# Kernel optimization log

Measured on AMD Instinct MI355X. Metric: run time of the kernel, lower is better.

Reference implementation:

```python
import jax, jax.numpy as jnp
import numpy as np


def setup_inputs() -> dict:
    key = jax.random.key(0)
    ks = jax.random.split(key, 8)
    B, T, V, D, H, C = 1024, 80, 50000, 300, 300, 3
    sent = jax.random.randint(ks[0], (B, T), 0, V, dtype=jnp.int32)
    lens = jax.random.randint(ks[1], (B,), 1, T + 1, dtype=jnp.int32)
    emb = jax.random.normal(ks[2], (V, D), dtype=jnp.float32) * 0.1
    Wx = jax.random.normal(ks[3], (D, 4 * H), dtype=jnp.float32) * 0.05
    Wh = jax.random.normal(ks[4], (H, 4 * H), dtype=jnp.float32) * 0.05
    b = jnp.zeros((4 * H,), dtype=jnp.float32)
    Wout = jax.random.normal(ks[5], (H, C), dtype=jnp.float32) * 0.05
    bout = jnp.zeros((C,), dtype=jnp.float32)
    return {"sent": sent, "lens": lens, "emb": emb, "Wx": Wx, "Wh": Wh,
            "b": b, "Wout": Wout, "bout": bout}


def _lstm_masked(x, mask, Wx, Wh, b, H):
    # x: [B, T, D], mask: [B, T] float. Scan over time keeping h,c in carry.
    B = x.shape[0]
    h0 = jnp.zeros((B, H), dtype=x.dtype)
    c0 = jnp.zeros((B, H), dtype=x.dtype)

    def step(carry, inp):
        h, c = carry
        xt, mt = inp                      # xt: [B, D], mt: [B]
        gates = xt @ Wx + h @ Wh + b      # [B, 4H]
        i, f, g, o = jnp.split(gates, 4, axis=-1)
        i, f, o = jax.nn.sigmoid(i), jax.nn.sigmoid(f), jax.nn.sigmoid(o)
        g = jnp.tanh(g)
        c_new = f * c + i * g
        h_new = o * jnp.tanh(c_new)
        m = mt[:, None]
        h = m * h_new + (1.0 - m) * h     # mask-based state blending
        c = m * c_new + (1.0 - m) * c
        return (h, c), None

    xs = (jnp.swapaxes(x, 0, 1), jnp.swapaxes(mask, 0, 1))  # time-major
    (h, c), _ = jax.lax.scan(step, (h0, c0), xs)
    return h


def reference(sent, lens, emb, Wx, Wh, b, Wout, bout):
    T = sent.shape[1]
    H = Wh.shape[0]
    x = emb[sent]                                         # [B, T, D]
    mask = (jnp.arange(T)[None, :] < lens[:, None]).astype(x.dtype)  # [B, T]
    h = _lstm_masked(x, mask, Wx, Wh, b, H)
    logit = h @ Wout + bout                               # [B, C]
    return logit
```

## Files before the change

### kernel.cpp

```cpp
#include <hip/hip_runtime.h>
#include <hip/hip_fp16.h>


typedef float    f32x4 __attribute__((ext_vector_type(4)));
typedef _Float16 f16;
typedef _Float16 f16x8 __attribute__((ext_vector_type(8)));
typedef unsigned long long u64;
typedef unsigned int       u32;

#define NB    1024
#define TT    80
#define NV    50000
#define ND    300
#define KP    320
#define NKT   10
#define SL    75
#define SLP   80
#define NTPG  5
#define NTIL  20
#define TPB   256
#define GRID  256

#define OFF_EMB   0
#define OFF_WHP   32000000
#define OFF_WXP   32819200
#define OFF_HBUF  33638400
#define HBUF_SZ   (NB * KP)
#define OFF_HF32  34949120
#define OFF_FLAGS 36177920
#define WS_NEED   36182016

__global__ __launch_bounds__(256) void absa_prep_emb(
    const float* __restrict__ emb, f16* __restrict__ embb) {
  int i = blockIdx.x * 256 + threadIdx.x;
  if (i >= NV * KP / 8) return;
  int flat = i * 8;
  int row  = flat / KP;
  int k    = flat - row * KP;
  f16x8 o;
  if (k + 7 < ND) {
    float4 a = *reinterpret_cast<const float4*>(emb + row * ND + k);
    float4 b = *reinterpret_cast<const float4*>(emb + row * ND + k + 4);
    o[0] = (f16)a.x; o[1] = (f16)a.y; o[2] = (f16)a.z; o[3] = (f16)a.w;
    o[4] = (f16)b.x; o[5] = (f16)b.y; o[6] = (f16)b.z; o[7] = (f16)b.w;
  } else {
#pragma unroll
    for (int e = 0; e < 8; ++e) {
      int kk = k + e;
      float v = (kk < ND) ? emb[row * ND + kk] : (kk == ND ? 1.0f : 0.0f);
      o[e] = (f16)v;
    }
  }
  *reinterpret_cast<f16x8*>(embb + flat) = o;
}

__global__ __launch_bounds__(256) void absa_prep_pack(
    const float* __restrict__ W, const float* __restrict__ bias,
    f16* __restrict__ out, int mode) {
  int idx = blockIdx.x * 256 + threadIdx.x;
  if (idx >= 4 * NTIL * NKT * 512) return;
  int e    = idx & 7;
  int lane = (idx >> 3) & 63;
  int fid  = idx >> 9;
  int kt   = fid % NKT;
  int rem  = fid / NKT;
  int nt   = rem % NTIL;
  int n    = rem / NTIL;
  int gi   = nt / NTPG, ti = nt - gi * NTPG;
  int k    = kt * 32 + (lane >> 4) * 8 + e;
  int cc   = ti * 16 + (lane & 15);
  float v = 0.f;
  if (cc < SL) {
    int col = gi * 300 + n * SL + cc;
    if (mode == 0) {
      if (k < ND)       v = W[k * 1200 + col];
      else if (k == ND) v = bias[col];
    } else {
      int kl = k % SLP, n2 = k / SLP;
      if (kl < SL)      v = W[(n2 * SL + kl) * 1200 + col];
    }
  }
  out[idx] = (f16)v;
}

__device__ __forceinline__ float sigf(float x) {
  return __builtin_amdgcn_rcpf(1.f + __builtin_amdgcn_exp2f(-1.44269504f * x));
}
__device__ __forceinline__ float tanhf_(float x) {
  float xx = fminf(15.f, fmaxf(-15.f, x));
  return 1.f - 2.f * __builtin_amdgcn_rcpf(1.f + __builtin_amdgcn_exp2f(2.88539008f * xx));
}

__global__ __launch_bounds__(TPB, 1) void absa_lstm(
    const int* __restrict__ sent, const int* __restrict__ lens,
    const f16* __restrict__ embb,
    const f16* __restrict__ whp, const f16* __restrict__ wxp,
    f16* __restrict__ hbuf, float* __restrict__ hf32,
    int* __restrict__ flags) {
  const int bid = blockIdx.x;
  const int s   = bid & 7;
  const int q   = bid >> 3;
  const int n   = q & 3;
  const int g   = s * 8 + (q >> 2);

  const int tid = threadIdx.x;
  const int w   = tid >> 6;
  const int l   = tid & 63;
  const int l15 = l & 15, lk = l >> 4;
  const int grow0 = g * 16;

  __shared__ float gates[4 * 80 * 20];
  __shared__ float c_lds[80 * 20];
  __shared__ float hf_lds[80 * 20];
  __shared__ int   sent_lds[16 * TT];
  __shared__ int   len_lds[16];

  for (int i = tid; i < 16 * TT; i += TPB) sent_lds[i] = sent[g * (16 * TT) + i];
  if (tid < 16) len_lds[tid] = lens[grow0 + tid];
  for (int i = tid; i < 80 * 20; i += TPB) { c_lds[i] = 0.f; hf_lds[i] = 0.f; }
  __syncthreads();

  int maxlen = 0;
#pragma unroll
  for (int r = 0; r < 16; ++r) maxlen = max(maxlen, len_lds[r]);

  f16x8 wh[NTPG][NKT], wx[NTPG][NKT];
#pragma unroll
  for (int j = 0; j < NTPG; ++j) {
#pragma unroll
    for (int kt = 0; kt < NKT; ++kt) {
      int off = ((n * NTIL + (w * NTPG + j)) * NKT + kt) * 512 + l * 8;
      wh[j][kt] = *reinterpret_cast<const f16x8*>(whp + off);
      wx[j][kt] = *reinterpret_cast<const f16x8*>(wxp + off);
    }
  }

  int gaddr[NTPG];
#pragma unroll
  for (int j = 0; j < NTPG; ++j)
    gaddr[j] = ((w * 80) + j * 16 + l15) * 20 + lk * 4;

  int* const flagp = flags + g * 16;

  for (int t = 0; t < TT; ++t) {
    if (t >= maxlen) break;

    f32x4 acc[NTPG];
#pragma unroll
    for (int j = 0; j < NTPG; ++j) acc[j] = (f32x4){0.f, 0.f, 0.f, 0.f};
    {
      f16x8 xa[NKT];
      const int srow = sent_lds[l15 * TT + t];
#pragma unroll
      for (int kt = 0; kt < NKT; ++kt)
        xa[kt] = *reinterpret_cast<const f16x8*>(embb + srow * KP + kt * 32 + lk * 8);
#pragma unroll
      for (int j = 0; j < NTPG; ++j)
#pragma unroll
        for (int kt = 0; kt < NKT; ++kt)
          acc[j] = __builtin_amdgcn_mfma_f32_16x16x32_f16(xa[kt], wx[j][kt], acc[j], 0, 0, 0);
    }

    if (t > 0) {
      {
        const int target = 4 * t;
        int spins = 0;
        while (__hip_atomic_load(flagp, __ATOMIC_RELAXED, __HIP_MEMORY_SCOPE_AGENT) < target
               && ++spins < (1 << 22))
          __builtin_amdgcn_s_sleep(1);
      }
      const f16* hp = hbuf + ((t - 1) & 1) * HBUF_SZ + (grow0 + l15) * KP;
      f16x8 ha[NKT];
#pragma unroll
      for (int kt = 0; kt < NKT; ++kt) {
        union { u64 qd[2]; f16x8 v; } u;
        const u64* p = reinterpret_cast<const u64*>(hp + kt * 32 + lk * 8);
        u.qd[0] = __hip_atomic_load(p,     __ATOMIC_RELAXED, __HIP_MEMORY_SCOPE_AGENT);
        u.qd[1] = __hip_atomic_load(p + 1, __ATOMIC_RELAXED, __HIP_MEMORY_SCOPE_AGENT);
        ha[kt] = u.v;
      }
#pragma unroll
      for (int j = 0; j < NTPG; ++j)
#pragma unroll
        for (int kt = 0; kt < NKT; ++kt)
          acc[j] = __builtin_amdgcn_mfma_f32_16x16x32_f16(ha[kt], wh[j][kt], acc[j], 0, 0, 0);
    }

#pragma unroll
    for (int j = 0; j < NTPG; ++j)
      *reinterpret_cast<f32x4*>(&gates[gaddr[j]]) = acc[j];
    __syncthreads();

    f16* hc = hbuf + (t & 1) * HBUF_SZ;
    for (int i = tid; i < 16 * 38; i += TPB) {
      int row = i & 15;
      int cc0 = (i >> 4) * 2;
      float hv[2];
#pragma unroll
      for (int e = 0; e < 2; ++e) {
        int cc = cc0 + e;
        float h = 0.f;
        if (cc < SL) {
          int base = cc * 20 + row;
          if (t < len_lds[row]) {
            float vi = gates[(0 * 80 + cc) * 20 + row];
            float vf = gates[(1 * 80 + cc) * 20 + row];
            float vg = gates[(2 * 80 + cc) * 20 + row];
            float vo = gates[(3 * 80 + cc) * 20 + row];
            float iv = sigf(vi), fv = sigf(vf), ov = sigf(vo);
            float gv = tanhf_(vg);
            float cn = fv * c_lds[base] + iv * gv;
            h = ov * tanhf_(cn);
            c_lds[base] = cn;
            hf_lds[base] = h;
          } else {
            h = hf_lds[base];
          }
        }
        hv[e] = h;
      }
      union { f16 h2[2]; u32 uu; } pu;
      pu.h2[0] = (f16)hv[0]; pu.h2[1] = (f16)hv[1];
      u32* dst = reinterpret_cast<u32*>(hc + (grow0 + row) * KP + n * SLP + cc0);
      __hip_atomic_store(dst, pu.uu, __ATOMIC_RELAXED, __HIP_MEMORY_SCOPE_AGENT);
    }
    __syncthreads();
    if (tid == 0)
      __hip_atomic_fetch_add(flagp, 1, __ATOMIC_RELAXED, __HIP_MEMORY_SCOPE_AGENT);
  }

  for (int i = tid; i < 16 * SL; i += TPB) {
    int row = i & 15, cc = i >> 4;
    hf32[(grow0 + row) * ND + n * SL + cc] = hf_lds[cc * 20 + row];
  }
}

__global__ __launch_bounds__(256) void absa_logits(
    const float* __restrict__ hf32, const float* __restrict__ Wout,
    const float* __restrict__ bout, float* __restrict__ out) {
  int row = blockIdx.x * 256 + threadIdx.x;
  if (row >= NB) return;
  float s0 = bout[0], s1 = bout[1], s2 = bout[2];
  for (int k = 0; k < ND; ++k) {
    float h = hf32[row * ND + k];
    s0 += h * Wout[k * 3 + 0];
    s1 += h * Wout[k * 3 + 1];
    s2 += h * Wout[k * 3 + 2];
  }
  out[row * 3 + 0] = s0;
  out[row * 3 + 1] = s1;
  out[row * 3 + 2] = s2;
}

extern "C" void kernel_launch(void* const* d_in, const int* in_sizes, int n_in,
                              void* d_out, int out_size, void* d_ws, size_t ws_size,
                              hipStream_t stream) {
  const int*   sent = (const int*)d_in[0];
  const int*   lens = (const int*)d_in[1];
  const float* emb  = (const float*)d_in[2];
  const float* Wx   = (const float*)d_in[3];
  const float* Wh   = (const float*)d_in[4];
  const float* bv   = (const float*)d_in[5];
  const float* Wout = (const float*)d_in[6];
  const float* bout = (const float*)d_in[7];
  float* out = (float*)d_out;

  char* wsb = (char*)d_ws;
  f16*   embb  = (f16*)(wsb + OFF_EMB);
  f16*   whp   = (f16*)(wsb + OFF_WHP);
  f16*   wxp   = (f16*)(wsb + OFF_WXP);
  f16*   hbuf  = (f16*)(wsb + OFF_HBUF);
  float* hf32  = (float*)(wsb + OFF_HF32);
  int*   flags = (int*)(wsb + OFF_FLAGS);

  (void)hipMemsetAsync(hbuf, 0, 2 * HBUF_SZ * 2, stream);
  (void)hipMemsetAsync(flags, 0, 64 * 64, stream);

  absa_prep_emb <<<(NV * KP / 8 + 255) / 256, 256, 0, stream>>>(emb, embb);
  absa_prep_pack<<<4 * NTIL * NKT * 512 / 256, 256, 0, stream>>>(Wh, bv, whp, 1);
  absa_prep_pack<<<4 * NTIL * NKT * 512 / 256, 256, 0, stream>>>(Wx, bv, wxp, 0);
  absa_lstm     <<<GRID, TPB, 0, stream>>>(sent, lens, embb, whp, wxp, hbuf, hf32, flags);
  absa_logits   <<<NB / 256, 256, 0, stream>>>(hf32, Wout, bout, out);
}
```

Before: 655.9 us.

## Replace flag counter sync with tagged h-buffer slabs and prefetch next x-projection

Removes the per-group atomic flag counter and instead embeds a step tag in the low mantissa bit of each f16 h value. Consumers spin directly on the data they need across 8 rotating buffer slabs, and gates are double-buffered in LDS so the second barrier per step can be dropped. The input projection for step t+1 is computed after h is published, taking it off the critical path, and Wx is now streamed from memory each step instead of held in registers. The two weight-pack launches are merged, and the logits kernel becomes a wave-per-row reduction. The tag bits slightly perturb h precision, and rereading Wx adds memory traffic.

```diff
diff --git a/kernel.cpp b/kernel.cpp
--- a/kernel.cpp
+++ b/kernel.cpp
@@ -20,15 +20,17 @@
 #define NTIL  20
 #define TPB   256
 #define GRID  256
+#define NSLAB 8
+
+#define TAGMASK 0x0001000100010001ULL
 
 #define OFF_EMB   0
 #define OFF_WHP   32000000
 #define OFF_WXP   32819200
 #define OFF_HBUF  33638400
 #define HBUF_SZ   (NB * KP)
-#define OFF_HF32  34949120
-#define OFF_FLAGS 36177920
-#define WS_NEED   36182016
+#define OFF_HF32  38881280
+#define WS_NEED   40110080
 
 __global__ __launch_bounds__(256) void absa_prep_emb(
     const float* __restrict__ emb, f16* __restrict__ embb) {
@@ -54,11 +56,15 @@
   *reinterpret_cast<f16x8*>(embb + flat) = o;
 }
 
-__global__ __launch_bounds__(256) void absa_prep_pack(
-    const float* __restrict__ W, const float* __restrict__ bias,
-    f16* __restrict__ out, int mode) {
-  int idx = blockIdx.x * 256 + threadIdx.x;
-  if (idx >= 4 * NTIL * NKT * 512) return;
+__global__ __launch_bounds__(256) void absa_prep_pack2(
+    const float* __restrict__ Wx, const float* __restrict__ Wh,
+    const float* __restrict__ bias,
+    f16* __restrict__ wxp, f16* __restrict__ whp) {
+  const int half = 4 * NTIL * NKT * 512;
+  int idx0 = blockIdx.x * 256 + threadIdx.x;
+  if (idx0 >= 2 * half) return;
+  int mode = idx0 >= half;
+  int idx  = idx0 - mode * half;
   int e    = idx & 7;
   int lane = (idx >> 3) & 63;
   int fid  = idx >> 9;
@@ -73,14 +79,14 @@
   if (cc < SL) {
     int col = gi * 300 + n * SL + cc;
     if (mode == 0) {
-      if (k < ND)       v = W[k * 1200 + col];
+      if (k < ND)       v = Wx[k * 1200 + col];
       else if (k == ND) v = bias[col];
     } else {
       int kl = k % SLP, n2 = k / SLP;
-      if (kl < SL)      v = W[(n2 * SL + kl) * 1200 + col];
-    }
-  }
-  out[idx] = (f16)v;
+      if (kl < SL)      v = Wh[(n2 * SL + kl) * 1200 + col];
+    }
+  }
+  (mode ? whp : wxp)[idx] = (f16)v;
 }
 
 __device__ __forceinline__ float sigf(float x) {
@@ -89,14 +95,18 @@
 __device__ __forceinline__ float tanhf_(float x) {
   float xx = fminf(15.f, fmaxf(-15.f, x));
   return 1.f - 2.f * __builtin_amdgcn_rcpf(1.f + __builtin_amdgcn_exp2f(2.88539008f * xx));
+}
+
+__device__ __forceinline__ u64 tag_pat(int tg) {
+  return ((u64)(tg & 1)) | ((u64)((tg >> 1) & 1) << 16) |
+         ((u64)((tg >> 2) & 1) << 32) | ((u64)((tg >> 3) & 1) << 48);
 }
 
 __global__ __launch_bounds__(TPB, 1) void absa_lstm(
     const int* __restrict__ sent, const int* __restrict__ lens,
     const f16* __restrict__ embb,
     const f16* __restrict__ whp, const f16* __restrict__ wxp,
-    f16* __restrict__ hbuf, float* __restrict__ hf32,
-    int* __restrict__ flags) {
+    f16* __restrict__ hbuf, float* __restrict__ hf32) {
   const int bid = blockIdx.x;
   const int s   = bid & 7;
   const int q   = bid >> 3;
@@ -109,13 +119,13 @@
   const int l15 = l & 15, lk = l >> 4;
   const int grow0 = g * 16;
 
-  __shared__ float gates[4 * 80 * 20];
+  __shared__ float gates[2 * 4 * 80 * 20];
   __shared__ float c_lds[80 * 20];
   __shared__ float hf_lds[80 * 20];
   __shared__ int   sent_lds[16 * TT];
   __shared__ int   len_lds[16];
 
-  for (int i = tid; i < 16 * TT; i += TPB) sent_lds[i] = sent[g * (16 * TT) + i];
+  for (int i = tid; i < 16 * TT; i += TPB) sent_lds[i] = sent[g * 16 * TT + i];
   if (tid < 16) len_lds[tid] = lens[grow0 + tid];
   for (int i = tid; i < 80 * 20; i += TPB) { c_lds[i] = 0.f; hf_lds[i] = 0.f; }
   __syncthreads();
@@ -124,111 +134,120 @@
 #pragma unroll
   for (int r = 0; r < 16; ++r) maxlen = max(maxlen, len_lds[r]);
 
-  f16x8 wh[NTPG][NKT], wx[NTPG][NKT];
-#pragma unroll
-  for (int j = 0; j < NTPG; ++j) {
-#pragma unroll
-    for (int kt = 0; kt < NKT; ++kt) {
-      int off = ((n * NTIL + (w * NTPG + j)) * NKT + kt) * 512 + l * 8;
-      wh[j][kt] = *reinterpret_cast<const f16x8*>(whp + off);
-      wx[j][kt] = *reinterpret_cast<const f16x8*>(wxp + off);
-    }
-  }
+  f16x8 wh[NTPG][NKT];
+#pragma unroll
+  for (int j = 0; j < NTPG; ++j)
+#pragma unroll
+    for (int kt = 0; kt < NKT; ++kt)
+      wh[j][kt] = *reinterpret_cast<const f16x8*>(
+          whp + ((size_t)(n * NTIL + (w * NTPG + j)) * NKT + kt) * 512 + l * 8);
 
   int gaddr[NTPG];
 #pragma unroll
   for (int j = 0; j < NTPG; ++j)
     gaddr[j] = ((w * 80) + j * 16 + l15) * 20 + lk * 4;
 
-  int* const flagp = flags + g * 16;
-
-  for (int t = 0; t < TT; ++t) {
-    if (t >= maxlen) break;
-
-    f32x4 acc[NTPG];
+  f32x4 acc[NTPG];
+
+  auto xpart = [&](int t) {
 #pragma unroll
     for (int j = 0; j < NTPG; ++j) acc[j] = (f32x4){0.f, 0.f, 0.f, 0.f};
+    f16x8 xa[NKT];
+    const int srow = sent_lds[l15 * TT + t];
+#pragma unroll
+    for (int kt = 0; kt < NKT; ++kt)
+      xa[kt] = *reinterpret_cast<const f16x8*>(embb + (size_t)srow * KP + kt * 32 + lk * 8);
+#pragma unroll
+    for (int j = 0; j < NTPG; ++j) {
+      f16x8 wxa[NKT];
+#pragma unroll
+      for (int kt = 0; kt < NKT; ++kt)
+        wxa[kt] = *reinterpret_cast<const f16x8*>(
+            wxp + ((size_t)(n * NTIL + (w * NTPG + j)) * NKT + kt) * 512 + l * 8);
+#pragma unroll
+      for (int kt = 0; kt < NKT; ++kt)
+        acc[j] = __builtin_amdgcn_mfma_f32_16x16x32_f16(xa[kt], wxa[kt], acc[j], 0, 0, 0);
+    }
+  };
+
+  xpart(0);
+
+  for (int t = 0; t < maxlen; ++t) {
+    const int par = (t & 1) * (4 * 80 * 20);
+
+    if (t > 0) {
+      const u64 expv = tag_pat((t - 1) % 15);
+      const f16* hp = hbuf + (size_t)((t - 1) & 7) * HBUF_SZ + (grow0 + l15) * KP + lk * 8;
+      u64 q0[NKT], q1[NKT];
+#pragma unroll
+      for (int kt = 0; kt < NKT; ++kt) {
+        const u64* p = reinterpret_cast<const u64*>(hp + kt * 32);
+        q0[kt] = __hip_atomic_load(p,     __ATOMIC_RELAXED, __HIP_MEMORY_SCOPE_AGENT);
+        q1[kt] = __hip_atomic_load(p + 1, __ATOMIC_RELAXED, __HIP_MEMORY_SCOPE_AGENT);
+      }
+#pragma unroll
+      for (int kt = 0; kt < NKT; ++kt) {
+        const u64* p = reinterpret_cast<const u64*>(hp + kt * 32);
+        int sp = 0;
+        while ((q0[kt] & TAGMASK) != expv && ++sp < (1 << 18))
+          q0[kt] = __hip_atomic_load(p,     __ATOMIC_RELAXED, __HIP_MEMORY_SCOPE_AGENT);
+        sp = 0;
+        while ((q1[kt] & TAGMASK) != expv && ++sp < (1 << 18))
+          q1[kt] = __hip_atomic_load(p + 1, __ATOMIC_RELAXED, __HIP_MEMORY_SCOPE_AGENT);
+        union { u64 qq[2]; f16x8 v; } u;
+        u.qq[0] = q0[kt]; u.qq[1] = q1[kt];
+#pragma unroll
+        for (int j = 0; j < NTPG; ++j)
+          acc[j] = __builtin_amdgcn_mfma_f32_16x16x32_f16(u.v, wh[j][kt], acc[j], 0, 0, 0);
+      }
+    }
+
+#pragma unroll
+    for (int j = 0; j < NTPG; ++j)
+      *reinterpret_cast<f32x4*>(&gates[par + gaddr[j]]) = acc[j];
+    __syncthreads();
+
     {
-      f16x8 xa[NKT];
-      const int srow = sent_lds[l15 * TT + t];
-#pragma unroll
-      for (int kt = 0; kt < NKT; ++kt)
-        xa[kt] = *reinterpret_cast<const f16x8*>(embb + srow * KP + kt * 32 + lk * 8);
-#pragma unroll
-      for (int j = 0; j < NTPG; ++j)
-#pragma unroll
-        for (int kt = 0; kt < NKT; ++kt)
-          acc[j] = __builtin_amdgcn_mfma_f32_16x16x32_f16(xa[kt], wx[j][kt], acc[j], 0, 0, 0);
-    }
-
-    if (t > 0) {
-      {
-        const int target = 4 * t;
-        int spins = 0;
-        while (__hip_atomic_load(flagp, __ATOMIC_RELAXED, __HIP_MEMORY_SCOPE_AGENT) < target
-               && ++spins < (1 << 22))
-          __builtin_amdgcn_s_sleep(1);
+      const u64 pat = tag_pat(t % 15);
+      f16* hc = hbuf + (size_t)(t & 7) * HBUF_SZ;
+      for (int i = tid; i < 320; i += TPB) {
+        int row = i & 15, qd = i >> 4;
+        union { unsigned short us[4]; u64 uu; } pu;
+#pragma unroll
+        for (int e = 0; e < 4; ++e) {
+          int cc = qd * 4 + e;
+          float h = 0.f;
+          if (cc < SL) {
+            int base = cc * 20 + row;
+            if (t < len_lds[row]) {
+              float vi = gates[par + (0 * 80 + cc) * 20 + row];
+              float vf = gates[par + (1 * 80 + cc) * 20 + row];
+              float vg = gates[par + (2 * 80 + cc) * 20 + row];
+              float vo = gates[par + (3 * 80 + cc) * 20 + row];
+              float iv = sigf(vi), fv = sigf(vf), ov = sigf(vo);
+              float gv = tanhf_(vg);
+              float cn = fv * c_lds[base] + iv * gv;
+              h = ov * tanhf_(cn);
+              c_lds[base] = cn;
+              hf_lds[base] = h;
+            } else {
+              h = hf_lds[base];
+            }
+          }
+          union { f16 f; unsigned short u; } cv;
+          cv.f = (f16)h;
+          pu.us[e] = cv.u;
+        }
+        pu.uu = (pu.uu & ~TAGMASK) | pat;
+        u64* dst = reinterpret_cast<u64*>(hc + (size_t)(grow0 + row) * KP + n * SLP + qd * 4);
+        __hip_atomic_store(dst, pu.uu, __ATOMIC_RELAXED, __HIP_MEMORY_SCOPE_AGENT);
       }
-      const f16* hp = hbuf + ((t - 1) & 1) * HBUF_SZ + (grow0 + l15) * KP;
-      f16x8 ha[NKT];
-#pragma unroll
-      for (int kt = 0; kt < NKT; ++kt) {
-        union { u64 qd[2]; f16x8 v; } u;
-        const u64* p = reinterpret_cast<const u64*>(hp + kt * 32 + lk * 8);
-        u.qd[0] = __hip_atomic_load(p,     __ATOMIC_RELAXED, __HIP_MEMORY_SCOPE_AGENT);
-        u.qd[1] = __hip_atomic_load(p + 1, __ATOMIC_RELAXED, __HIP_MEMORY_SCOPE_AGENT);
-        ha[kt] = u.v;
-      }
-#pragma unroll
-      for (int j = 0; j < NTPG; ++j)
-#pragma unroll
-        for (int kt = 0; kt < NKT; ++kt)
-          acc[j] = __builtin_amdgcn_mfma_f32_16x16x32_f16(ha[kt], wh[j][kt], acc[j], 0, 0, 0);
-    }
-
-#pragma unroll
-    for (int j = 0; j < NTPG; ++j)
-      *reinterpret_cast<f32x4*>(&gates[gaddr[j]]) = acc[j];
-    __syncthreads();
-
-    f16* hc = hbuf + (t & 1) * HBUF_SZ;
-    for (int i = tid; i < 16 * 38; i += TPB) {
-      int row = i & 15;
-      int cc0 = (i >> 4) * 2;
-      float hv[2];
-#pragma unroll
-      for (int e = 0; e < 2; ++e) {
-        int cc = cc0 + e;
-        float h = 0.f;
-        if (cc < SL) {
-          int base = cc * 20 + row;
-          if (t < len_lds[row]) {
-            float vi = gates[(0 * 80 + cc) * 20 + row];
-            float vf = gates[(1 * 80 + cc) * 20 + row];
-            float vg = gates[(2 * 80 + cc) * 20 + row];
-            float vo = gates[(3 * 80 + cc) * 20 + row];
-            float iv = sigf(vi), fv = sigf(vf), ov = sigf(vo);
-            float gv = tanhf_(vg);
-            float cn = fv * c_lds[base] + iv * gv;
-            h = ov * tanhf_(cn);
-            c_lds[base] = cn;
-            hf_lds[base] = h;
-          } else {
-            h = hf_lds[base];
-          }
-        }
-        hv[e] = h;
-      }
-      union { f16 h2[2]; u32 uu; } pu;
-      pu.h2[0] = (f16)hv[0]; pu.h2[1] = (f16)hv[1];
-      u32* dst = reinterpret_cast<u32*>(hc + (grow0 + row) * KP + n * SLP + cc0);
-      __hip_atomic_store(dst, pu.uu, __ATOMIC_RELAXED, __HIP_MEMORY_SCOPE_AGENT);
-    }
-    __syncthreads();
-    if (tid == 0)
-      __hip_atomic_fetch_add(flagp, 1, __ATOMIC_RELAXED, __HIP_MEMORY_SCOPE_AGENT);
-  }
-
+    }
+
+    if (t + 1 < maxlen) xpart(t + 1);
+  }
+
+  __syncthreads();
   for (int i = tid; i < 16 * SL; i += TPB) {
     int row = i & 15, cc = i >> 4;
     hf32[(grow0 + row) * ND + n * SL + cc] = hf_lds[cc * 20 + row];
@@ -238,18 +257,26 @@
 __global__ __launch_bounds__(256) void absa_logits(
     const float* __restrict__ hf32, const float* __restrict__ Wout,
     const float* __restrict__ bout, float* __restrict__ out) {
-  int row = blockIdx.x * 256 + threadIdx.x;
-  if (row >= NB) return;
-  float s0 = bout[0], s1 = bout[1], s2 = bout[2];
-  for (int k = 0; k < ND; ++k) {
-    float h = hf32[row * ND + k];
+  int row = blockIdx.x * 4 + (threadIdx.x >> 6);
+  int l   = threadIdx.x & 63;
+  float s0 = 0.f, s1 = 0.f, s2 = 0.f;
+  for (int k = l; k < ND; k += 64) {
+    float h  = hf32[row * ND + k];
     s0 += h * Wout[k * 3 + 0];
     s1 += h * Wout[k * 3 + 1];
     s2 += h * Wout[k * 3 + 2];
   }
-  out[row * 3 + 0] = s0;
-  out[row * 3 + 1] = s1;
-  out[row * 3 + 2] = s2;
+#pragma unroll
+  for (int o = 32; o; o >>= 1) {
+    s0 += __shfl_down(s0, o);
+    s1 += __shfl_down(s1, o);
+    s2 += __shfl_down(s2, o);
+  }
+  if (l == 0) {
+    out[row * 3 + 0] = s0 + bout[0];
+    out[row * 3 + 1] = s1 + bout[1];
+    out[row * 3 + 2] = s2 + bout[2];
+  }
 }
 
 extern "C" void kernel_launch(void* const* d_in, const int* in_sizes, int n_in,
@@ -266,19 +293,16 @@
   float* out = (float*)d_out;
 
   char* wsb = (char*)d_ws;
-  f16*   embb  = (f16*)(wsb + OFF_EMB);
-  f16*   whp   = (f16*)(wsb + OFF_WHP);
-  f16*   wxp   = (f16*)(wsb + OFF_WXP);
-  f16*   hbuf  = (f16*)(wsb + OFF_HBUF);
-  float* hf32  = (float*)(wsb + OFF_HF32);
-  int*   flags = (int*)(wsb + OFF_FLAGS);
-
-  (void)hipMemsetAsync(hbuf, 0, 2 * HBUF_SZ * 2, stream);
-  (void)hipMemsetAsync(flags, 0, 64 * 64, stream);
-
-  absa_prep_emb <<<(NV * KP / 8 + 255) / 256, 256, 0, stream>>>(emb, embb);
-  absa_prep_pack<<<4 * NTIL * NKT * 512 / 256, 256, 0, stream>>>(Wh, bv, whp, 1);
-  absa_prep_pack<<<4 * NTIL * NKT * 512 / 256, 256, 0, stream>>>(Wx, bv, wxp, 0);
-  absa_lstm     <<<GRID, TPB, 0, stream>>>(sent, lens, embb, whp, wxp, hbuf, hf32, flags);
-  absa_logits   <<<NB / 256, 256, 0, stream>>>(hf32, Wout, bout, out);
-}
+  f16*   embb = (f16*)(wsb + OFF_EMB);
+  f16*   whp  = (f16*)(wsb + OFF_WHP);
+  f16*   wxp  = (f16*)(wsb + OFF_WXP);
+  f16*   hbuf = (f16*)(wsb + OFF_HBUF);
+  float* hf32 = (float*)(wsb + OFF_HF32);
+
+  (void)hipMemsetAsync(hbuf, 0xFF, NSLAB * NB * KP * 2, stream);
+
+  absa_prep_emb  <<<(NV * KP / 8 + 255) / 256, 256, 0, stream>>>(emb, embb);
+  absa_prep_pack2<<<2 * 4 * NTIL * NKT * 512 / 256, 256, 0, stream>>>(Wx, Wh, bv, wxp, whp);
+  absa_lstm      <<<GRID, TPB, 0, stream>>>(sent, lens, embb, whp, wxp, hbuf, hf32);
+  absa_logits    <<<NB / 4, 256, 0, stream>>>(hf32, Wout, bout, out);
+}
```

Measured after the change: 758.6 us. 1.16x slower.
